# Kernel tuning notes

Measured on AMD Instinct MI355X. Metric: run time of the kernel, lower is better.

Reference implementation:

```python
import jax, jax.numpy as jnp
import numpy as np

B, C, H, W = 512, 64, 32, 64
NUM_NODE = 128


def setup_inputs() -> dict:
    key = jax.random.key(0)
    ks = jax.random.split(key, 11)
    f = jnp.float32
    def nrm(k, shape, s):
        return jax.random.normal(k, shape, f) * s
    return {
        "x":   jax.random.normal(ks[0], (B, C, H, W), f),
        "w11": nrm(ks[1], (32, 64, 1, 1), 0.1), "b11": nrm(ks[2], (32,), 0.05),
        "w12": nrm(ks[3], (16, 32, 3, 3), 0.1), "b12": nrm(ks[4], (16,), 0.05),
        "w21": nrm(ks[5], (8, 16, 1, 1), 0.1),  "b21": nrm(ks[6], (8,), 0.05),
        "w22": nrm(ks[7], (4, 8, 3, 3), 0.1),   "b22": nrm(ks[8], (4,), 0.05),
        "fcw": nrm(ks[9], (2 * NUM_NODE, 32 * 64 * 4), 0.05),
        "fcb": nrm(ks[10], (2 * NUM_NODE,), 0.05),
    }


def _conv_relu(x, w, b, pad):
    y = jax.lax.conv_general_dilated(
        x, w, window_strides=(1, 1), padding=[(pad, pad), (pad, pad)],
        dimension_numbers=("NCHW", "OIHW", "NCHW"))
    return jax.nn.relu(y + b[None, :, None, None])


def reference(x, w11, b11, w12, b12, w21, b21, w22, b22, fcw, fcb):
    # --- GraphGen3: conv stack -> fc -> n_Sigmoid -> [B, N, 2] ---
    h = _conv_relu(x, w11, b11, 0)
    h = _conv_relu(h, w12, b12, 1)
    h = _conv_relu(h, w21, b21, 0)
    h = _conv_relu(h, w22, b22, 1)          # [B, 4, 32, 64]
    z = h.reshape(h.shape[0], -1) @ fcw.T + fcb  # [B, 2N]
    c01 = jax.nn.sigmoid(3.0 * z).reshape(x.shape[0], -1, 2)  # n_Sigmoid(x, 3)
    # --- get_coord: scale normalized coords to pixel range ---
    Hd, Wd = x.shape[2], x.shape[3]
    coord = c01 * jnp.array([Hd - 1, Wd - 1], x.dtype)  # [B, N, 2]
    # --- th_batch_map_coordinates: clamp, corner gather, bilinear lerp ---
    ch = jnp.clip(coord[..., 0], 0.0, Hd - 1)
    cw = jnp.clip(coord[..., 1], 0.0, Wd - 1)
    h0 = jnp.floor(ch).astype(jnp.int32); h1 = jnp.ceil(ch).astype(jnp.int32)
    w0 = jnp.floor(cw).astype(jnp.int32); w1 = jnp.ceil(cw).astype(jnp.int32)
    bidx = jnp.arange(x.shape[0])[:, None]  # [B, 1]
    def gv(hi, wi):
        return x[bidx, :, hi, wi]           # gather -> [B, N, C]
    v_lt = gv(h0, w0); v_rt = gv(h1, w0)
    v_lb = gv(h0, w1); v_rb = gv(h1, w1)
    oh = (ch - h0.astype(x.dtype))[..., None]
    ow = (cw - w0.astype(x.dtype))[..., None]
    vt = v_lt + oh * (v_rt - v_lt)
    vb = v_lb + oh * (v_rb - v_lb)
    graph_feat = vt + ow * (vb - vt)        # [B, N, C] (matches permute(0,2,1))
    return graph_feat, coord
```

## Files before the change

### kernel.cpp

```cpp
#include <hip/hip_runtime.h>
#include <hip/hip_fp16.h>
#include <cstdint>

#define BATCH 512
#define CIN   64
#define HH    32
#define WW    64
#define HW    2048
#define C1    32
#define C2    16
#define C3    8
#define C4    4
#define NOUT  256
#define KFC   8192
#define NODES 128
#define KS    16
#define GF_SIZE (BATCH * NODES * CIN)

typedef __attribute__((ext_vector_type(8))) short bfrag;
typedef __attribute__((ext_vector_type(4))) float ffrag;

__device__ __forceinline__ ushort bf_trunc(float f) { return (ushort)(__float_as_uint(f) >> 16); }
__device__ __forceinline__ float  bf_truncf(float f) { return __uint_as_float(__float_as_uint(f) & 0xffff0000u); }
__device__ __forceinline__ ushort f2bf(float f) {
  uint32_t u = __float_as_uint(f);
  return (ushort)((u + 0x7fffu + ((u >> 16) & 1u)) >> 16);
}
__device__ __forceinline__ uint32_t pack2(float a, float b) {
  return (uint32_t)f2bf(a) | ((uint32_t)f2bf(b) << 16);
}
__device__ __forceinline__ uint32_t packhi2(float a, float b) {
  return (uint32_t)bf_trunc(a) | ((uint32_t)bf_trunc(b) << 16);
}
__device__ __forceinline__ ushort f2h(float f) { return __half_as_ushort(__float2half_rn(f)); }
__device__ __forceinline__ uint32_t packh2(float a, float b) {
  return (uint32_t)f2h(a) | ((uint32_t)f2h(b) << 16);
}
__device__ __forceinline__ float h2f(uint32_t u) { return __half2float(__ushort_as_half((ushort)u)); }
__device__ __forceinline__ float bf2f(ushort u) { return __uint_as_float(((uint32_t)u) << 16); }

__global__ __launch_bounds__(256) void k_xpose(
    const float* __restrict__ x, ushort* __restrict__ xt)
{
  __shared__ uint32_t tb[256 * 33];
  const int t  = threadIdx.x;
  const int b  = blockIdx.y;
  const int rg = blockIdx.x;
  const float* xp = x + (size_t)b * CIN * HW + rg * 256 + t;
  #pragma unroll
  for (int j = 0; j < 32; ++j) {
    float v0 = xp[(size_t)(2 * j) * HW];
    float v1 = xp[(size_t)(2 * j + 1) * HW];
    tb[t * 33 + j] = pack2(v0, v1);
  }
  __syncthreads();
  ushort* op = xt + ((size_t)b * HW + rg * 256) * CIN;
  #pragma unroll
  for (int k = 0; k < 8; ++k) {
    const int u = k * 256 + t;
    const int p = u >> 3, q = u & 7;
    uint4 v;
    v.x = tb[p * 33 + q * 4 + 0];
    v.y = tb[p * 33 + q * 4 + 1];
    v.z = tb[p * 33 + q * 4 + 2];
    v.w = tb[p * 33 + q * 4 + 3];
    *(uint4*)(op + (size_t)u * 8) = v;
  }
}

__global__ __launch_bounds__(256) void k_conv12(
    const ushort* __restrict__ xt, const float* __restrict__ w11, const float* __restrict__ b11,
    const float* __restrict__ w12, const float* __restrict__ b12,
    ushort* __restrict__ h2, int b0)
{
  __shared__ __align__(16) char h1s[10 * 66 * 64];
  const int tid = threadIdx.x;
  const int l   = tid & 63;
  const int wv  = tid >> 6;
  const int lr  = l & 15;
  const int lg  = l >> 4;
  const int r0  = blockIdx.x * 8;
  const int bg  = b0 + blockIdx.y;
  const ushort* xtb = xt + (size_t)bg * HW * CIN;

  if (tid < 160) {
    int row = tid >> 4, half = (tid >> 3) & 1, q = tid & 7;
    int cell = row * 66 + (half ? 65 : 0);
    *(uint2*)(h1s + (cell << 6) + q * 8) = uint2{0u, 0u};
  }

  bfrag w1h[2][2], w1l[2][2];
  #pragma unroll
  for (int m = 0; m < 2; ++m) {
    #pragma unroll
    for (int ks = 0; ks < 2; ++ks) {
      const float* wp = w11 + (m * 16 + lr) * 64 + ks * 32 + lg * 8;
      #pragma unroll
      for (int e = 0; e < 8; ++e) {
        float v = wp[e];
        w1h[m][ks][e] = (short)bf_trunc(v);
        w1l[m][ks][e] = (short)f2bf(v - bf_truncf(v));
      }
    }
  }
  float bias1[2][4];
  #pragma unroll
  for (int m = 0; m < 2; ++m) {
    #pragma unroll
    for (int r = 0; r < 4; ++r) bias1[m][r] = b11[m * 16 + lg * 4 + r];
  }

  auto ldfrag = [&](int nt, bfrag& f0, bfrag& f1) {
    const int ry = nt >> 2, col0 = (nt & 3) << 4;
    const int y  = r0 - 1 + ry;
    if (y >= 0 && y < HH) {
      const ushort* xp = xtb + (size_t)(y * WW + col0 + lr) * CIN + lg * 8;
      f0 = *(const bfrag*)xp;
      f1 = *(const bfrag*)(xp + 32);
    } else {
      #pragma unroll
      for (int e = 0; e < 8; ++e) { f0[e] = 0; f1[e] = 0; }
    }
  };
  auto comp = [&](int nt, bfrag f0, bfrag f1) {
    const int ry = nt >> 2, col0 = (nt & 3) << 4;
    const int y  = r0 - 1 + ry;
    const bool valid = (y >= 0) && (y < HH);
    const int colb = col0 + 1 + lr;
    ffrag a0 = {0.f, 0.f, 0.f, 0.f}, a1 = {0.f, 0.f, 0.f, 0.f};
    a0 = __builtin_amdgcn_mfma_f32_16x16x32_bf16(w1h[0][0], f0, a0, 0, 0, 0);
    a0 = __builtin_amdgcn_mfma_f32_16x16x32_bf16(w1l[0][0], f0, a0, 0, 0, 0);
    a0 = __builtin_amdgcn_mfma_f32_16x16x32_bf16(w1h[0][1], f1, a0, 0, 0, 0);
    a0 = __builtin_amdgcn_mfma_f32_16x16x32_bf16(w1l[0][1], f1, a0, 0, 0, 0);
    a1 = __builtin_amdgcn_mfma_f32_16x16x32_bf16(w1h[1][0], f0, a1, 0, 0, 0);
    a1 = __builtin_amdgcn_mfma_f32_16x16x32_bf16(w1l[1][0], f0, a1, 0, 0, 0);
    a1 = __builtin_amdgcn_mfma_f32_16x16x32_bf16(w1h[1][1], f1, a1, 0, 0, 0);
    a1 = __builtin_amdgcn_mfma_f32_16x16x32_bf16(w1l[1][1], f1, a1, 0, 0, 0);
    #pragma unroll
    for (int m = 0; m < 2; ++m) {
      uint2 sv;
      if (valid) {
        float v0 = fmaxf((m ? a1[0] : a0[0]) + bias1[m][0], 0.f);
        float v1 = fmaxf((m ? a1[1] : a0[1]) + bias1[m][1], 0.f);
        float v2 = fmaxf((m ? a1[2] : a0[2]) + bias1[m][2], 0.f);
        float v3 = fmaxf((m ? a1[3] : a0[3]) + bias1[m][3], 0.f);
        sv = uint2{pack2(v0, v1), pack2(v2, v3)};
      } else {
        sv = uint2{0u, 0u};
      }
      int chunk = (m * 2 + (lg >> 1)) ^ ((colb >> 1) & 3);
      char* dst = h1s + ((ry * 66 + colb) << 6) + (chunk << 4) + (lg & 1) * 8;
      *(uint2*)dst = sv;
    }
  };

  {
    bfrag c0, c1, n0, n1;
    ldfrag(wv * 10 + 0, c0, c1);
    #pragma unroll
    for (int i = 0; i < 10; ++i) {
      if (i < 9) ldfrag(wv * 10 + i + 1, n0, n1);
      comp(wv * 10 + i, c0, c1);
      c0 = n0; c1 = n1;
    }
  }
  __syncthreads();

  bfrag w2h[9], w2l[9];
  #pragma unroll
  for (int t = 0; t < 9; ++t) {
    const float* wp = w12 + lr * 288 + t;
    #pragma unroll
    for (int e = 0; e < 8; ++e) {
      float v = wp[(lg * 8 + e) * 9];
      w2h[t][e] = (short)bf_trunc(v);
      w2l[t][e] = (short)f2bf(v - bf_truncf(v));
    }
  }
  float bias2[4];
  #pragma unroll
  for (int r = 0; r < 4; ++r) bias2[r] = b12[lg * 4 + r];

  #pragma unroll 2
  for (int i = 0; i < 8; ++i) {
    const int nt   = wv * 8 + i;
    const int ryo  = nt >> 2;
    const int col0 = (nt & 3) << 4;
    ffrag acc = {0.f, 0.f, 0.f, 0.f};
    #pragma unroll
    for (int ky = 0; ky < 3; ++ky) {
      const int row = ryo + ky;
      #pragma unroll
      for (int kx = 0; kx < 3; ++kx) {
        const int colb  = col0 + lr + kx;
        const int chunk = lg ^ ((colb >> 1) & 3);
        const bfrag hv = *(const bfrag*)(h1s + ((row * 66 + colb) << 6) + (chunk << 4));
        acc = __builtin_amdgcn_mfma_f32_16x16x32_bf16(w2h[ky * 3 + kx], hv, acc, 0, 0, 0);
        acc = __builtin_amdgcn_mfma_f32_16x16x32_bf16(w2l[ky * 3 + kx], hv, acc, 0, 0, 0);
      }
    }
    const int px = (r0 + ryo) * WW + col0 + lr;
    uint2 o;
    o.x = packh2(fmaxf(acc[0] + bias2[0], 0.f), fmaxf(acc[1] + bias2[1], 0.f));
    o.y = packh2(fmaxf(acc[2] + bias2[2], 0.f), fmaxf(acc[3] + bias2[3], 0.f));
    *(uint2*)(h2 + ((size_t)blockIdx.y * HW + px) * 16 + lg * 4) = o;
  }
}

__global__ __launch_bounds__(256) void k_conv34(
    const ushort* __restrict__ h2, const float* __restrict__ w21, const float* __restrict__ b21,
    const float* __restrict__ w22, const float* __restrict__ b22,
    ushort* __restrict__ h4h, ushort* __restrict__ h4l)
{
  __shared__ float h3s[18][64][9];
  __shared__ float __align__(16) w21s[128];
  __shared__ float __align__(16) w22s[288];
  const int tid = threadIdx.x;
  const int r0  = blockIdx.x * 16;
  const size_t b = blockIdx.y;

  for (int i = tid; i < 128; i += 256) w21s[(i & 15) * 8 + (i >> 4)] = w21[i];
  for (int i = tid; i < 288; i += 256) {
    int o = i / 72, r = i - o * 72, c = r / 9, tap = r - c * 9;
    w22s[(tap * 8 + c) * 4 + o] = w22[i];
  }
  __syncthreads();

  for (int p = tid; p < 18 * 64; p += 256) {
    const int ry = p >> 6, wc = p & 63;
    const int y  = r0 - 1 + ry;
    float* hd = &h3s[ry][wc][0];
    if (y >= 0 && y < HH) {
      const uint4* hp = (const uint4*)(h2 + ((b * HH + y) * WW + wc) * 16);
      uint4 ua = hp[0], ub = hp[1];
      uint32_t uw[8] = {ua.x, ua.y, ua.z, ua.w, ub.x, ub.y, ub.z, ub.w};
      float xv[16];
      #pragma unroll
      for (int j = 0; j < 8; ++j) {
        xv[2*j]   = h2f(uw[j] & 0xffffu);
        xv[2*j+1] = h2f(uw[j] >> 16);
      }
      float acc[C3];
      #pragma unroll
      for (int o = 0; o < C3; ++o) acc[o] = b21[o];
      #pragma unroll
      for (int c = 0; c < 16; ++c) {
        const float4* wr = (const float4*)&w21s[c * 8];
        float4 a = wr[0], d = wr[1];
        float v = xv[c];
        acc[0] = fmaf(v, a.x, acc[0]); acc[1] = fmaf(v, a.y, acc[1]);
        acc[2] = fmaf(v, a.z, acc[2]); acc[3] = fmaf(v, a.w, acc[3]);
        acc[4] = fmaf(v, d.x, acc[4]); acc[5] = fmaf(v, d.y, acc[5]);
        acc[6] = fmaf(v, d.z, acc[6]); acc[7] = fmaf(v, d.w, acc[7]);
      }
      #pragma unroll
      for (int c = 0; c < C3; ++c) hd[c] = fmaxf(acc[c], 0.f);
    } else {
      #pragma unroll
      for (int c = 0; c < C3; ++c) hd[c] = 0.f;
    }
  }
  __syncthreads();

  for (int p = tid; p < 1024; p += 256) {
    const int yl = p >> 6, wc = p & 63, ry = yl + 1;
    float acc[C4] = {b22[0], b22[1], b22[2], b22[3]};
    #pragma unroll
    for (int ky = 0; ky < 3; ++ky) {
      #pragma unroll
      for (int kx = 0; kx < 3; ++kx) {
        const int wcc = wc + kx - 1;
        if (wcc < 0 || wcc >= WW) continue;
        const float* hb = &h3s[ry + ky - 1][wcc][0];
        const int tap = ky * 3 + kx;
        #pragma unroll
        for (int c = 0; c < C3; ++c) {
          float v = hb[c];
          float4 w4 = *(const float4*)&w22s[(tap * 8 + c) * 4];
          acc[0] = fmaf(v, w4.x, acc[0]); acc[1] = fmaf(v, w4.y, acc[1]);
          acc[2] = fmaf(v, w4.z, acc[2]); acc[3] = fmaf(v, w4.w, acc[3]);
        }
      }
    }
    const size_t base = b * KFC + (r0 + yl) * WW + wc;
    #pragma unroll
    for (int o = 0; o < C4; ++o) {
      float v = fmaxf(acc[o], 0.f);
      h4h[base + (size_t)o * HW] = bf_trunc(v);
      h4l[base + (size_t)o * HW] = f2bf(v - bf_truncf(v));
    }
  }
}

__global__ __launch_bounds__(256) void k_cvt_fcw(
    const float* __restrict__ w, ushort* __restrict__ hi, ushort* __restrict__ lo)
{
  const int i = (blockIdx.x * 256 + threadIdx.x) * 8;
  const float4 a = *(const float4*)(w + i);
  const float4 b = *(const float4*)(w + i + 4);
  uint4 hv, lv;
  hv.x = packhi2(a.x, a.y); hv.y = packhi2(a.z, a.w);
  hv.z = packhi2(b.x, b.y); hv.w = packhi2(b.z, b.w);
  lv.x = pack2(a.x - bf_truncf(a.x), a.y - bf_truncf(a.y));
  lv.y = pack2(a.z - bf_truncf(a.z), a.w - bf_truncf(a.w));
  lv.z = pack2(b.x - bf_truncf(b.x), b.y - bf_truncf(b.y));
  lv.w = pack2(b.z - bf_truncf(b.z), b.w - bf_truncf(b.w));
  *(uint4*)(hi + i) = hv;
  *(uint4*)(lo + i) = lv;
}

__global__ __launch_bounds__(256) void k_fc(
    const ushort* __restrict__ Ahp, const ushort* __restrict__ Alp,
    const ushort* __restrict__ Bhp, const ushort* __restrict__ Blp,
    float* __restrict__ zpart, int cb)
{
  const int tid = threadIdx.x;
  const int l   = tid & 63;
  const int wv  = tid >> 6;
  const int lr  = l & 15;
  const int lg  = l >> 4;
  const int m0  = blockIdx.x * 64 + (wv >> 1) * 32;
  const int n0  = blockIdx.y * 64 + (wv & 1) * 32;
  const int k0  = blockIdx.z * (KFC / KS);

  int mrow[2], nrow[2];
  #pragma unroll
  for (int t = 0; t < 2; ++t) {
    int m = m0 + t * 16 + lr;
    mrow[t] = m < cb ? m : cb - 1;
    nrow[t] = n0 + t * 16 + lr;
  }
  ffrag acc[2][2] = {};

  #pragma unroll 1
  for (int kc = 0; kc < (KFC / KS) / 32; ++kc) {
    const int k = k0 + kc * 32 + lg * 8;
    bfrag ah[2], al[2], bh[2], bl[2];
    #pragma unroll
    for (int t = 0; t < 2; ++t) {
      ah[t] = *(const bfrag*)(Ahp + (size_t)mrow[t] * KFC + k);
      al[t] = *(const bfrag*)(Alp + (size_t)mrow[t] * KFC + k);
      bh[t] = *(const bfrag*)(Bhp + (size_t)nrow[t] * KFC + k);
      bl[t] = *(const bfrag*)(Blp + (size_t)nrow[t] * KFC + k);
    }
    #pragma unroll
    for (int mt = 0; mt < 2; ++mt) {
      #pragma unroll
      for (int nt = 0; nt < 2; ++nt) {
        acc[mt][nt] = __builtin_amdgcn_mfma_f32_16x16x32_bf16(ah[mt], bh[nt], acc[mt][nt], 0, 0, 0);
        acc[mt][nt] = __builtin_amdgcn_mfma_f32_16x16x32_bf16(ah[mt], bl[nt], acc[mt][nt], 0, 0, 0);
        acc[mt][nt] = __builtin_amdgcn_mfma_f32_16x16x32_bf16(al[mt], bh[nt], acc[mt][nt], 0, 0, 0);
      }
    }
  }

  #pragma unroll
  for (int mt = 0; mt < 2; ++mt) {
    #pragma unroll
    for (int r = 0; r < 4; ++r) {
      const int m = m0 + mt * 16 + lg * 4 + r;
      if (m < cb) {
        #pragma unroll
        for (int nt = 0; nt < 2; ++nt)
          zpart[((size_t)blockIdx.z * cb + m) * NOUT + n0 + nt * 16 + lr] = acc[mt][nt][r];
      }
    }
  }
}

__global__ __launch_bounds__(256) void k_gather(
    const ushort* __restrict__ xt, const float* __restrict__ zpart,
    const float* __restrict__ fcb, float* __restrict__ out, int cb, int b0)
{
  const int bid = blockIdx.x;
  int bl, g;
  if ((cb & 7) == 0) {
    const int xcd = bid & 7;
    const int j   = bid >> 3;
    g  = j & 31;
    bl = (j >> 5) * 8 + xcd;
  } else {
    bl = bid >> 5;
    g  = bid & 31;
  }
  const int node = g * 4 + (threadIdx.x >> 6);
  const int l    = threadIdx.x & 63;
  const int bg   = b0 + bl;

  float val = 0.f;
  if (l < 2 * KS) {
    const int kb = l >> 1, comp = l & 1;
    val = zpart[((size_t)kb * cb + bl) * NOUT + node * 2 + comp];
  }
  #pragma unroll
  for (int off = 2; off < 2 * KS; off <<= 1) val += __shfl_xor(val, off);
  const float z0 = __shfl(val, 0) + fcb[node * 2 + 0];
  const float z1 = __shfl(val, 1) + fcb[node * 2 + 1];
  const float ch = 31.f / (1.f + __expf(-3.f * z0));
  const float cw = 63.f / (1.f + __expf(-3.f * z1));

  if (l < 2)
    out[GF_SIZE + (((size_t)bg * NODES + node) << 1) + l] = l ? cw : ch;

  const float chv = fminf(fmaxf(ch, 0.f), 31.f);
  const float cwv = fminf(fmaxf(cw, 0.f), 63.f);
  const float fh = floorf(chv), fw = floorf(cwv);
  const int h0 = (int)fh, h1i = (int)ceilf(chv);
  const int w0 = (int)fw, w1i = (int)ceilf(cwv);
  const float oh = chv - fh, ow = cwv - fw;
  const ushort* xbp = xt + (size_t)bg * HW * CIN + l;
  const float v_lt = bf2f(xbp[(size_t)(h0 * WW + w0) * CIN]);
  const float v_rt = bf2f(xbp[(size_t)(h1i * WW + w0) * CIN]);
  const float v_lb = bf2f(xbp[(size_t)(h0 * WW + w1i) * CIN]);
  const float v_rb = bf2f(xbp[(size_t)(h1i * WW + w1i) * CIN]);
  const float vt = v_lt + oh * (v_rt - v_lt);
  const float vb = v_lb + oh * (v_rb - v_lb);
  out[((size_t)bg * NODES + node) * CIN + l] = vt + ow * (vb - vt);
}

extern "C" void kernel_launch(void* const* d_in, const int* in_sizes, int n_in,
                              void* d_out, int out_size, void* d_ws, size_t ws_size,
                              hipStream_t stream)
{
  (void)in_sizes; (void)n_in; (void)out_size;
  const float* x   = (const float*)d_in[0];
  const float* w11 = (const float*)d_in[1];
  const float* b11 = (const float*)d_in[2];
  const float* w12 = (const float*)d_in[3];
  const float* b12 = (const float*)d_in[4];
  const float* w21 = (const float*)d_in[5];
  const float* b21 = (const float*)d_in[6];
  const float* w22 = (const float*)d_in[7];
  const float* b22 = (const float*)d_in[8];
  const float* fcw = (const float*)d_in[9];
  const float* fcb = (const float*)d_in[10];
  float* out = (float*)d_out;
  char* wsb  = (char*)d_ws;

  const size_t xtBytes = (size_t)BATCH * HW * CIN * 2;
  const size_t perB    = 65536 + 16384 + 16384 + (size_t)KS * NOUT * 4;
  const size_t fixed   = xtBytes + 2 * 4194304;
  size_t avail = ws_size > fixed ? ws_size - fixed : perB;
  size_t cbmax = avail / perB;
  int CB = (int)(cbmax < (size_t)BATCH ? cbmax : (size_t)BATCH);
  if (CB < 1) CB = 1;

  char* p = wsb;
  ushort* xtv  = (ushort*)p;  p += xtBytes;
  ushort* h2v  = (ushort*)p;  p += (size_t)CB * 65536;
  ushort* h4h  = (ushort*)p;  p += (size_t)CB * 16384;
  ushort* h4l  = (ushort*)p;  p += (size_t)CB * 16384;
  float*  zpv  = (float*)p;   p += (size_t)CB * KS * NOUT * 4;
  ushort* fcwh = (ushort*)p;  p += 4194304;
  ushort* fcwl = (ushort*)p;

  k_cvt_fcw<<<dim3(NOUT * KFC / (256 * 8)), 256, 0, stream>>>(fcw, fcwh, fcwl);
  k_xpose<<<dim3(8, BATCH), 256, 0, stream>>>(x, xtv);

  for (int b0 = 0; b0 < BATCH; b0 += CB) {
    const int cb = (BATCH - b0 < CB) ? (BATCH - b0) : CB;
    k_conv12<<<dim3(4, cb), 256, 0, stream>>>(xtv, w11, b11, w12, b12, h2v, b0);
    k_conv34<<<dim3(2, cb), 256, 0, stream>>>(h2v, w21, b21, w22, b22, h4h, h4l);
    k_fc<<<dim3((cb + 63) / 64, 4, KS), 256, 0, stream>>>(h4h, h4l, fcwh, fcwl, zpv, cb);
    k_gather<<<dim3(cb * 32), 256, 0, stream>>>(xtv, zpv, fcb, out, cb, b0);
  }
}
```

Baseline: 234.8 us.

## Fuse conv1-2 and conv3-4 into one kernel with halo recomputation in LDS

Merges the conv12 and conv34 kernels into one. Each block now computes a 12-row conv1 tile and a 10-row conv2 tile (recomputing halo rows), keeps the fp16 conv2 output in shared memory, then runs conv3 and conv4 on 8 output rows. This removes the global h2 intermediate round trip and one kernel launch. The cost is redundant halo computation for conv1 and conv2, and conv3/conv4 weights now read directly from global/scalar memory instead of LDS.

```diff
diff --git a/kernel.cpp b/kernel.cpp
--- a/kernel.cpp
+++ b/kernel.cpp
@@ -68,12 +68,14 @@
   }
 }
 
-__global__ __launch_bounds__(256) void k_conv12(
+__global__ __launch_bounds__(256) void k_conv1234(
     const ushort* __restrict__ xt, const float* __restrict__ w11, const float* __restrict__ b11,
     const float* __restrict__ w12, const float* __restrict__ b12,
-    ushort* __restrict__ h2, int b0)
-{
-  __shared__ __align__(16) char h1s[10 * 66 * 64];
+    const float* __restrict__ w21, const float* __restrict__ b21,
+    const float* __restrict__ w22, const float* __restrict__ b22,
+    ushort* __restrict__ h4h, ushort* __restrict__ h4l, int b0)
+{
+  __shared__ __align__(16) char smem[12 * 66 * 64];
   const int tid = threadIdx.x;
   const int l   = tid & 63;
   const int wv  = tid >> 6;
@@ -83,10 +85,10 @@
   const int bg  = b0 + blockIdx.y;
   const ushort* xtb = xt + (size_t)bg * HW * CIN;
 
-  if (tid < 160) {
-    int row = tid >> 4, half = (tid >> 3) & 1, q = tid & 7;
-    int cell = row * 66 + (half ? 65 : 0);
-    *(uint2*)(h1s + (cell << 6) + q * 8) = uint2{0u, 0u};
+  if (tid < 192) {
+    int cell = tid >> 3, q = tid & 7;
+    int row = cell >> 1, colb = (cell & 1) ? 65 : 0;
+    *(uint2*)(smem + ((row * 66 + colb) << 6) + q * 8) = uint2{0u, 0u};
   }
 
   bfrag w1h[2][2], w1l[2][2];
@@ -112,7 +114,7 @@
 
   auto ldfrag = [&](int nt, bfrag& f0, bfrag& f1) {
     const int ry = nt >> 2, col0 = (nt & 3) << 4;
-    const int y  = r0 - 1 + ry;
+    const int y  = r0 - 2 + ry;
     if (y >= 0 && y < HH) {
       const ushort* xp = xtb + (size_t)(y * WW + col0 + lr) * CIN + lg * 8;
       f0 = *(const bfrag*)xp;
@@ -124,7 +126,7 @@
   };
   auto comp = [&](int nt, bfrag f0, bfrag f1) {
     const int ry = nt >> 2, col0 = (nt & 3) << 4;
-    const int y  = r0 - 1 + ry;
+    const int y  = r0 - 2 + ry;
     const bool valid = (y >= 0) && (y < HH);
     const int colb = col0 + 1 + lr;
     ffrag a0 = {0.f, 0.f, 0.f, 0.f}, a1 = {0.f, 0.f, 0.f, 0.f};
@@ -149,18 +151,18 @@
         sv = uint2{0u, 0u};
       }
       int chunk = (m * 2 + (lg >> 1)) ^ ((colb >> 1) & 3);
-      char* dst = h1s + ((ry * 66 + colb) << 6) + (chunk << 4) + (lg & 1) * 8;
+      char* dst = smem + ((ry * 66 + colb) << 6) + (chunk << 4) + (lg & 1) * 8;
       *(uint2*)dst = sv;
     }
   };
 
   {
     bfrag c0, c1, n0, n1;
-    ldfrag(wv * 10 + 0, c0, c1);
-    #pragma unroll
-    for (int i = 0; i < 10; ++i) {
-      if (i < 9) ldfrag(wv * 10 + i + 1, n0, n1);
-      comp(wv * 10 + i, c0, c1);
+    ldfrag(wv * 12 + 0, c0, c1);
+    #pragma unroll
+    for (int i = 0; i < 12; ++i) {
+      if (i < 11) ldfrag(wv * 12 + i + 1, n0, n1);
+      comp(wv * 12 + i, c0, c1);
       c0 = n0; c1 = n1;
     }
   }
@@ -181,58 +183,47 @@
   #pragma unroll
   for (int r = 0; r < 4; ++r) bias2[r] = b12[lg * 4 + r];
 
-  #pragma unroll 2
-  for (int i = 0; i < 8; ++i) {
-    const int nt   = wv * 8 + i;
-    const int ryo  = nt >> 2;
+  uint32_t ph0[10], ph1[10];
+  #pragma unroll
+  for (int i = 0; i < 10; ++i) {
+    const int nt   = wv * 10 + i;
+    const int hryo = nt >> 2;
     const int col0 = (nt & 3) << 4;
     ffrag acc = {0.f, 0.f, 0.f, 0.f};
     #pragma unroll
     for (int ky = 0; ky < 3; ++ky) {
-      const int row = ryo + ky;
+      const int row = hryo + ky;
       #pragma unroll
       for (int kx = 0; kx < 3; ++kx) {
         const int colb  = col0 + lr + kx;
         const int chunk = lg ^ ((colb >> 1) & 3);
-        const bfrag hv = *(const bfrag*)(h1s + ((row * 66 + colb) << 6) + (chunk << 4));
+        const bfrag hv = *(const bfrag*)(smem + ((row * 66 + colb) << 6) + (chunk << 4));
         acc = __builtin_amdgcn_mfma_f32_16x16x32_bf16(w2h[ky * 3 + kx], hv, acc, 0, 0, 0);
         acc = __builtin_amdgcn_mfma_f32_16x16x32_bf16(w2l[ky * 3 + kx], hv, acc, 0, 0, 0);
       }
     }
-    const int px = (r0 + ryo) * WW + col0 + lr;
-    uint2 o;
-    o.x = packh2(fmaxf(acc[0] + bias2[0], 0.f), fmaxf(acc[1] + bias2[1], 0.f));
-    o.y = packh2(fmaxf(acc[2] + bias2[2], 0.f), fmaxf(acc[3] + bias2[3], 0.f));
-    *(uint2*)(h2 + ((size_t)blockIdx.y * HW + px) * 16 + lg * 4) = o;
-  }
-}
-
-__global__ __launch_bounds__(256) void k_conv34(
-    const ushort* __restrict__ h2, const float* __restrict__ w21, const float* __restrict__ b21,
-    const float* __restrict__ w22, const float* __restrict__ b22,
-    ushort* __restrict__ h4h, ushort* __restrict__ h4l)
-{
-  __shared__ float h3s[18][64][9];
-  __shared__ float __align__(16) w21s[128];
-  __shared__ float __align__(16) w22s[288];
-  const int tid = threadIdx.x;
-  const int r0  = blockIdx.x * 16;
-  const size_t b = blockIdx.y;
-
-  for (int i = tid; i < 128; i += 256) w21s[(i & 15) * 8 + (i >> 4)] = w21[i];
-  for (int i = tid; i < 288; i += 256) {
-    int o = i / 72, r = i - o * 72, c = r / 9, tap = r - c * 9;
-    w22s[(tap * 8 + c) * 4 + o] = w22[i];
+    ph0[i] = packh2(fmaxf(acc[0] + bias2[0], 0.f), fmaxf(acc[1] + bias2[1], 0.f));
+    ph1[i] = packh2(fmaxf(acc[2] + bias2[2], 0.f), fmaxf(acc[3] + bias2[3], 0.f));
   }
   __syncthreads();
 
-  for (int p = tid; p < 18 * 64; p += 256) {
+  #pragma unroll
+  for (int i = 0; i < 10; ++i) {
+    const int nt   = wv * 10 + i;
+    const int hryo = nt >> 2;
+    const int col  = ((nt & 3) << 4) + lr;
+    *(uint2*)(smem + ((hryo * 64 + col) << 5) + lg * 8) = uint2{ph0[i], ph1[i]};
+  }
+  __syncthreads();
+
+  float* h3b = (float*)(smem + 20480);
+  for (int p = tid; p < 640; p += 256) {
     const int ry = p >> 6, wc = p & 63;
     const int y  = r0 - 1 + ry;
-    float* hd = &h3s[ry][wc][0];
+    float* hd = h3b + (ry * 64 + wc) * 9;
     if (y >= 0 && y < HH) {
-      const uint4* hp = (const uint4*)(h2 + ((b * HH + y) * WW + wc) * 16);
-      uint4 ua = hp[0], ub = hp[1];
+      const uint4 ua = *(const uint4*)(smem + ((ry * 64 + wc) << 5));
+      const uint4 ub = *(const uint4*)(smem + ((ry * 64 + wc) << 5) + 16);
       uint32_t uw[8] = {ua.x, ua.y, ua.z, ua.w, ub.x, ub.y, ub.z, ub.w};
       float xv[16];
       #pragma unroll
@@ -245,13 +236,10 @@
       for (int o = 0; o < C3; ++o) acc[o] = b21[o];
       #pragma unroll
       for (int c = 0; c < 16; ++c) {
-        const float4* wr = (const float4*)&w21s[c * 8];
-        float4 a = wr[0], d = wr[1];
         float v = xv[c];
-        acc[0] = fmaf(v, a.x, acc[0]); acc[1] = fmaf(v, a.y, acc[1]);
-        acc[2] = fmaf(v, a.z, acc[2]); acc[3] = fmaf(v, a.w, acc[3]);
-        acc[4] = fmaf(v, d.x, acc[4]); acc[5] = fmaf(v, d.y, acc[5]);
-        acc[6] = fmaf(v, d.z, acc[6]); acc[7] = fmaf(v, d.w, acc[7]);
+        #pragma unroll
+        for (int o = 0; o < C3; ++o)
+          acc[o] = fmaf(v, w21[o * 16 + c], acc[o]);
       }
       #pragma unroll
       for (int c = 0; c < C3; ++c) hd[c] = fmaxf(acc[c], 0.f);
@@ -262,8 +250,8 @@
   }
   __syncthreads();
 
-  for (int p = tid; p < 1024; p += 256) {
-    const int yl = p >> 6, wc = p & 63, ry = yl + 1;
+  for (int p = tid; p < 512; p += 256) {
+    const int yl = p >> 6, wc = p & 63;
     float acc[C4] = {b22[0], b22[1], b22[2], b22[3]};
     #pragma unroll
     for (int ky = 0; ky < 3; ++ky) {
@@ -271,18 +259,18 @@
       for (int kx = 0; kx < 3; ++kx) {
         const int wcc = wc + kx - 1;
         if (wcc < 0 || wcc >= WW) continue;
-        const float* hb = &h3s[ry + ky - 1][wcc][0];
+        const float* hb = h3b + ((yl + ky) * 64 + wcc) * 9;
         const int tap = ky * 3 + kx;
         #pragma unroll
         for (int c = 0; c < C3; ++c) {
           float v = hb[c];
-          float4 w4 = *(const float4*)&w22s[(tap * 8 + c) * 4];
-          acc[0] = fmaf(v, w4.x, acc[0]); acc[1] = fmaf(v, w4.y, acc[1]);
-          acc[2] = fmaf(v, w4.z, acc[2]); acc[3] = fmaf(v, w4.w, acc[3]);
+          #pragma unroll
+          for (int o = 0; o < C4; ++o)
+            acc[o] = fmaf(v, w22[(o * 8 + c) * 9 + tap], acc[o]);
         }
       }
     }
-    const size_t base = b * KFC + (r0 + yl) * WW + wc;
+    const size_t base = (size_t)blockIdx.y * KFC + (r0 + yl) * WW + wc;
     #pragma unroll
     for (int o = 0; o < C4; ++o) {
       float v = fmaxf(acc[o], 0.f);
@@ -438,7 +426,7 @@
   char* wsb  = (char*)d_ws;
 
   const size_t xtBytes = (size_t)BATCH * HW * CIN * 2;
-  const size_t perB    = 65536 + 16384 + 16384 + (size_t)KS * NOUT * 4;
+  const size_t perB    = 16384 + 16384 + (size_t)KS * NOUT * 4;
   const size_t fixed   = xtBytes + 2 * 4194304;
   size_t avail = ws_size > fixed ? ws_size - fixed : perB;
   size_t cbmax = avail / perB;
@@ -447,7 +435,6 @@
 
   char* p = wsb;
   ushort* xtv  = (ushort*)p;  p += xtBytes;
-  ushort* h2v  = (ushort*)p;  p += (size_t)CB * 65536;
   ushort* h4h  = (ushort*)p;  p += (size_t)CB * 16384;
   ushort* h4l  = (ushort*)p;  p += (size_t)CB * 16384;
   float*  zpv  = (float*)p;   p += (size_t)CB * KS * NOUT * 4;
@@ -459,8 +446,8 @@
 
   for (int b0 = 0; b0 < BATCH; b0 += CB) {
     const int cb = (BATCH - b0 < CB) ? (BATCH - b0) : CB;
-    k_conv12<<<dim3(4, cb), 256, 0, stream>>>(xtv, w11, b11, w12, b12, h2v, b0);
-    k_conv34<<<dim3(2, cb), 256, 0, stream>>>(h2v, w21, b21, w22, b22, h4h, h4l);
+    k_conv1234<<<dim3(4, cb), 256, 0, stream>>>(xtv, w11, b11, w12, b12,
+                                                w21, b21, w22, b22, h4h, h4l, b0);
     k_fc<<<dim3((cb + 63) / 64, 4, KS), 256, 0, stream>>>(h4h, h4l, fcwh, fcwl, zpv, cb);
     k_gather<<<dim3(cb * 32), 256, 0, stream>>>(xtv, zpv, fcb, out, cb, b0);
   }
```

After: 225.2 us. 1.04x faster.
